# Optimization experiments

Measured on AMD Instinct MI355X. Metric: run time of the kernel, lower is better.

The kernel has to match this reference:

```python
import jax, jax.numpy as jnp
import numpy as np

N, E, R, D = 50000, 640000, 200, 128  # nodes, edges, relations, feat dim (in_feat==out_feat)
EPS = 1e-5  # LayerNorm eps
NEG_SLOPE = 0.01  # F.leaky_relu default

def _xavier(k, shape):
    gain = np.sqrt(2.0)  # calculate_gain('relu')
    std = gain * np.sqrt(2.0 / (shape[0] + shape[1]))
    a = np.sqrt(3.0) * std
    return jax.random.uniform(k, shape, jnp.float32, -a, a)

def setup_inputs() -> dict:
    key = jax.random.key(0)
    ks = jax.random.split(key, 10)
    return {
        "node": jax.random.normal(ks[0], (N, D), jnp.float32),
        "rel": jax.random.normal(ks[1], (R, D), jnp.float32),
        "norm": jax.random.uniform(ks[2], (N, 1), jnp.float32),
        "w_triplet": _xavier(ks[3], (3 * D, D)),
        "w_quad": _xavier(ks[4], (D, D)),
        "loop_weight": _xavier(ks[5], (D, D)),
        "evolve_loop_weight": _xavier(ks[6], (D, D)),
        "src": jax.random.randint(ks[7], (E,), 0, N),
        "dst": jax.random.randint(ks[8], (E,), 0, N),
        "etype": jax.random.randint(ks[9], (E,), 0, R),
    }

def reference(node, rel, norm, w_triplet, w_quad, loop_weight, evolve_loop_weight, src, dst, etype):
    # triplet = cat([h_src, rel_emb, h_dst], 1) @ w_triplet, computed blockwise
    # to avoid materializing the [E, 3D] concat.
    W_s, W_r, W_d = w_triplet[:D], w_triplet[D:2 * D], w_triplet[2 * D:]
    triplet = node[src] @ W_s + rel[etype] @ W_r + node[dst] @ W_d  # [E, D]
    # 'fre' not in edata -> sro_fre is zeros; a_triplet = triplet @ w_quad
    a = jax.nn.leaky_relu(triplet @ w_quad, negative_slope=NEG_SLOPE)  # [E, D]
    # edge_softmax: softmax over incoming edges per destination node, per feature
    a_max = jax.ops.segment_max(a, dst, num_segments=N)
    a_max = jnp.where(jnp.isfinite(a_max), a_max, 0.0)  # empty segments -> -inf
    ex = jnp.exp(a - a_max[dst])
    denom = jax.ops.segment_sum(ex, dst, num_segments=N)
    att = ex / denom[dst]
    # weighted scatter-sum aggregation, then apply_func: h * norm
    h = jax.ops.segment_sum(att * triplet, dst, num_segments=N) * norm  # [N, D]
    # self-loop: evolve_loop_weight for in-degree-0 nodes, loop_weight otherwise
    indeg = jax.ops.segment_sum(jnp.ones((E,), jnp.float32), dst, num_segments=N)
    loop = jnp.where((indeg > 0)[:, None], node @ loop_weight, node @ evolve_loop_weight)
    out = h + loop
    # LayerNorm(elementwise_affine=False)
    mu = jnp.mean(out, axis=-1, keepdims=True)
    var = jnp.var(out, axis=-1, keepdims=True)
    return (out - mu) * jax.lax.rsqrt(var + EPS)
```

## Files before the change

kernel.cpp:

```cpp
#include <hip/hip_runtime.h>
#include <hip/hip_bf16.h>

#define D 128

typedef __attribute__((ext_vector_type(8))) short bf16x8;
typedef __attribute__((ext_vector_type(4))) float f32x4;

__device__ __forceinline__ unsigned short f2bf_bits(float f) {
    union { __hip_bfloat16 h; unsigned short u; } c;
    c.h = __float2bfloat16(f);
    return c.u;
}
__device__ __forceinline__ float bfbits2f(unsigned short u) {
    return __uint_as_float(((unsigned)u) << 16);
}
__device__ __forceinline__ float ldf(const void* p, size_t i, int f32) {
    return f32 ? ((const float*)p)[i] : bfbits2f(((const unsigned short*)p)[i]);
}
__device__ __forceinline__ void unpk(unsigned u, float& a, float& b) {
    a = __uint_as_float(u << 16);
    b = __uint_as_float(u & 0xFFFF0000u);
}

__global__ void init_kernel(const void* node, int* flag, int* a, int n) {
    if (blockIdx.x == 0 && threadIdx.x < 64) {
        int t = threadIdx.x;
        int bad = 0;
        for (int j = 0; j < 4; j++) {
            float v = bfbits2f(((const unsigned short*)node)[t + 64 * j]);
            if (!(fabsf(v) < 1e4f)) bad = 1;
        }
        unsigned long long m = __ballot(bad);
        if (t == 0) *flag = (m != 0ull) ? 1 : 0;
    }
    int i = blockIdx.x * blockDim.x + threadIdx.x;
    int s = gridDim.x * blockDim.x;
    for (int j = i; j < n; j += s) a[j] = 0;
}

__global__ void wq_kernel(const void* w_trip, const void* w_quad,
                          unsigned short* wsqAll, const int* flag) {
    int f32 = *flag;
    int k = blockIdx.x, m = blockIdx.y, t = threadIdx.x;
    float acc = 0.f;
    for (int j = 0; j < D; j++)
        acc += ldf(w_trip, (size_t)m * D * D + (size_t)k * D + j, f32) *
               ldf(w_quad, (size_t)j * D + t, f32);
    wsqAll[m * D * D + k * D + t] = f2bf_bits(acc);
}

__global__ void trans_kernel(const void* wtrip, const void* loopW, const void* evoW,
                             const unsigned short* wsqAll, unsigned short* wT,
                             const int* flag) {
    int j = blockIdx.x;
    int f32 = *flag;
    const void* srcp; size_t base; int isbf;
    switch (j) {
        case 0: srcp = wsqAll; base = 0;         isbf = 1;    break;
        case 1: srcp = wtrip;  base = 0;         isbf = !f32; break;
        case 2: srcp = wsqAll; base = 2 * D * D; isbf = 1;    break;
        case 3: srcp = wtrip;  base = 2 * D * D; isbf = !f32; break;
        case 4: srcp = loopW;  base = 0;         isbf = !f32; break;
        case 5: srcp = evoW;   base = 0;         isbf = !f32; break;
        case 6: srcp = wsqAll; base = D * D;     isbf = 1;    break;
        default: srcp = wtrip; base = D * D;     isbf = !f32; break;
    }
    for (int c = threadIdx.x; c < 1024; c += blockDim.x) {
        int idx = blockIdx.y * 1024 + c;
        int n = idx >> 7, k = idx & 127;
        unsigned short b;
        if (isbf) b = ((const unsigned short*)srcp)[base + (size_t)k * D + n];
        else      b = f2bf_bits(((const float*)srcp)[base + (size_t)k * D + n]);
        wT[(size_t)j * D * D + (size_t)n * D + k] = b;
    }
}

__global__ __launch_bounds__(256) void gemm_kernel(
    const void* __restrict__ node, const void* __restrict__ rel,
    const unsigned short* __restrict__ wT, const int* __restrict__ cnt,
    unsigned* __restrict__ nodeST, unsigned* __restrict__ nodeDT,
    unsigned* __restrict__ relRT, unsigned* __restrict__ loopSel,
    const int* __restrict__ flag, int N, int R, int nodeBlocks) {
    __shared__ __align__(16) unsigned short Wt[D][D + 8];

    int f32 = *flag;
    int bx = blockIdx.x;
    int isRel = bx >= nodeBlocks;
    int jp = isRel ? 3 : blockIdx.y;
    if (isRel && blockIdx.y != 0) return;

    int rows = isRel ? R : N;
    int row0 = (isRel ? bx - nodeBlocks : bx) * 64;
    const void* A = isRel ? rel : node;

    int tid = threadIdx.y * 64 + threadIdx.x;
    int lane = threadIdx.x, wv = threadIdx.y;
    int l16 = lane & 15, quad = lane >> 4;
    int ar = row0 + wv * 16 + l16;
    int ar_c = ar < rows ? ar : rows - 1;

    int qIdx, tIdx;
    unsigned* O = nullptr;
    switch (jp) {
        case 0: qIdx = 0; tIdx = 1; O = nodeST; break;
        case 1: qIdx = 2; tIdx = 3; O = nodeDT; break;
        case 2: qIdx = 4; tIdx = 5; break;
        default: qIdx = 6; tIdx = 7; O = relRT; break;
    }

    bf16x8 af[4];
#pragma unroll
    for (int kk = 0; kk < 4; kk++) {
        int k = kk * 32 + quad * 8;
        if (f32) {
            const float* Af = (const float*)A + (size_t)ar_c * D + k;
#pragma unroll
            for (int j = 0; j < 8; j++) af[kk][j] = (short)f2bf_bits(Af[j]);
        } else {
            af[kk] = *(const bf16x8*)((const unsigned short*)A + (size_t)ar_c * D + k);
        }
    }

    const unsigned short* gQ = wT + (size_t)qIdx * D * D;
    const unsigned short* gT = wT + (size_t)tIdx * D * D;

    bf16x8 wreg[8], wreg2[8];
#pragma unroll
    for (int i = 0; i < 8; i++) {
        int c = tid + i * 256;
        wreg[i] = *(const bf16x8*)(gQ + (c >> 4) * 128 + (c & 15) * 8);
    }

    f32x4 accQ[8], accT[8];
#pragma unroll
    for (int i = 0; i < 8; i++) {
        accQ[i] = (f32x4){0.f, 0.f, 0.f, 0.f};
        accT[i] = (f32x4){0.f, 0.f, 0.f, 0.f};
    }

    for (int pass = 0; pass < 2; pass++) {
#pragma unroll
        for (int i = 0; i < 8; i++) {
            int c = tid + i * 256;
            *(bf16x8*)(&Wt[c >> 4][(c & 15) * 8]) = wreg[i];
        }
        if (pass == 0) {
#pragma unroll
            for (int i = 0; i < 8; i++) {
                int c = tid + i * 256;
                wreg2[i] = *(const bf16x8*)(gT + (c >> 4) * 128 + (c & 15) * 8);
            }
        }
        __syncthreads();
        f32x4* acc = pass ? accT : accQ;
#pragma unroll
        for (int kk = 0; kk < 4; kk++) {
#pragma unroll
            for (int nt = 0; nt < 8; nt++) {
                bf16x8 bfr = *(const bf16x8*)(&Wt[nt * 16 + l16][kk * 32 + quad * 8]);
                acc[nt] = __builtin_amdgcn_mfma_f32_16x16x32_bf16(af[kk], bfr, acc[nt], 0, 0, 0);
            }
        }
        __syncthreads();
#pragma unroll
        for (int i = 0; i < 8; i++) wreg[i] = wreg2[i];
    }

    int cr0 = row0 + wv * 16 + quad * 4;
    int odd = l16 & 1;
    if (jp != 2) {
#pragma unroll
        for (int r = 0; r < 4; r++) {
            int cr = cr0 + r;
#pragma unroll
            for (int nt = 0; nt < 8; nt++) {
                float vQ = accQ[nt][r], vT = accT[nt][r];
                float oQ = __shfl_xor(vQ, 1);
                float oT = __shfl_xor(vT, 1);
                unsigned w;
                if (!odd) w = (unsigned)f2bf_bits(vQ) | ((unsigned)f2bf_bits(oQ) << 16);
                else      w = (unsigned)f2bf_bits(oT) | ((unsigned)f2bf_bits(vT) << 16);
                if (cr < rows) O[(size_t)cr * 128 + nt * 16 + l16] = w;
            }
        }
    } else {
#pragma unroll
        for (int r = 0; r < 4; r++) {
            int cr = cr0 + r;
            int deg = (cr < rows) ? cnt[cr] : 0;
#pragma unroll
            for (int nt = 0; nt < 8; nt++) {
                float vL = accQ[nt][r], vE = accT[nt][r];
                float oL = __shfl_xor(vL, 1);
                float oE = __shfl_xor(vE, 1);
                unsigned wl, we;
                if (!odd) {
                    wl = (unsigned)f2bf_bits(vL) | ((unsigned)f2bf_bits(oL) << 16);
                    we = (unsigned)f2bf_bits(vE) | ((unsigned)f2bf_bits(oE) << 16);
                } else {
                    wl = (unsigned)f2bf_bits(oL) | ((unsigned)f2bf_bits(vL) << 16);
                    we = (unsigned)f2bf_bits(oE) | ((unsigned)f2bf_bits(vE) << 16);
                }
                if (cr < rows && !odd)
                    loopSel[(size_t)cr * 64 + nt * 8 + (l16 >> 1)] = (deg > 0) ? wl : we;
            }
        }
    }
}

__global__ void count_kernel(const int* __restrict__ dst, int* __restrict__ cnt, int E) {
    int e = blockIdx.x * blockDim.x + threadIdx.x;
    if (e < E) atomicAdd(&cnt[dst[e]], 1);
}

__global__ void scan_block(const int* __restrict__ cnt, int* __restrict__ offs,
                           int* __restrict__ part, int N) {
    __shared__ int sh[256];
    int tid = threadIdx.x;
    int i = blockIdx.x * 256 + tid;
    int v = (i < N) ? cnt[i] : 0;
    sh[tid] = v;
    __syncthreads();
    for (int o = 1; o < 256; o <<= 1) {
        int t = (tid >= o) ? sh[tid - o] : 0;
        __syncthreads();
        sh[tid] += t;
        __syncthreads();
    }
    if (i < N) offs[i] = sh[tid] - v;
    if (tid == 255) part[blockIdx.x] = sh[255];
}

__global__ void scan_part(int* __restrict__ part, int nb) {
    __shared__ int sh[256];
    int tid = threadIdx.x;
    int v = (tid < nb) ? part[tid] : 0;
    sh[tid] = v;
    __syncthreads();
    for (int o = 1; o < 256; o <<= 1) {
        int t = (tid >= o) ? sh[tid - o] : 0;
        __syncthreads();
        sh[tid] += t;
        __syncthreads();
    }
    if (tid < nb) part[tid] = sh[tid] - v;
}

__global__ void scan_add(int* __restrict__ offs, const int* __restrict__ part,
                         int N, int E) {
    int i = blockIdx.x * 256 + threadIdx.x;
    if (i < N) offs[i] += part[blockIdx.x];
    if (i == 0) offs[N] = E;
}

__global__ void scatter_kernel(const int* __restrict__ src, const int* __restrict__ dst,
                               const int* __restrict__ et, const int* __restrict__ offs,
                               int* __restrict__ cur, unsigned* __restrict__ ePack, int E) {
    int e = blockIdx.x * blockDim.x + threadIdx.x;
    if (e >= E) return;
    int d = dst[e];
    int pos = offs[d] + atomicAdd(&cur[d], 1);
    ePack[pos] = (unsigned)src[e] | ((unsigned)et[e] << 20);
}

__global__ __launch_bounds__(256) void agg_kernel(
    const int* __restrict__ offs, const unsigned* __restrict__ ePack,
    const uint2* __restrict__ ST, const uint2* __restrict__ RT,
    const uint2* __restrict__ DT, const unsigned* __restrict__ loopSel,
    const void* __restrict__ normv, void* __restrict__ out,
    const int* __restrict__ flag, int N) {
    int n = blockIdx.x * 4 + threadIdx.y;
    if (n >= N) return;
    int f32 = *flag;
    int lane = threadIdx.x;
    int start = offs[n], end = offs[n + 1];
    int deg = end - start;

    unsigned ul = loopSel[(size_t)n * 64 + lane];
    uint2 ud = DT[(size_t)n * 64 + lane];
    float qd0, qd1, td0, td1, acc0, acc1;
    unpk(ud.x, qd0, qd1);
    unpk(ud.y, td0, td1);
    unpk(ul, acc0, acc1);

    float den0 = 0.f, den1 = 0.f, h0 = 0.f, h1 = 0.f;
    for (int e0 = start; e0 < end; e0 += 64) {
        int m = end - e0;
        if (m > 64) m = 64;
        unsigned pk = (lane < m) ? ePack[e0 + lane] : 0u;
        int j = 0;
#define EDGE_LOADS(J, US, UR)                                         \
        unsigned pk_##US = __shfl(pk, (J));                           \
        uint2 US = ST[(size_t)(pk_##US & 0xFFFFFu) * 64 + lane];      \
        uint2 UR = RT[(size_t)(pk_##US >> 20) * 64 + lane];
#define EDGE_MATH(US, UR)                                             \
        {                                                             \
            float qs0, qs1, qr0, qr1, ts0, ts1, tr0, tr1;             \
            unpk(US.x, qs0, qs1); unpk(UR.x, qr0, qr1);               \
            unpk(US.y, ts0, ts1); unpk(UR.y, tr0, tr1);               \
            float q0 = qs0 + qr0 + qd0, q1 = qs1 + qr1 + qd1;         \
            float a0 = q0 > 0.f ? q0 : 0.01f * q0;                    \
            float a1 = q1 > 0.f ? q1 : 0.01f * q1;                    \
            float ex0 = __expf(a0), ex1 = __expf(a1);                 \
            den0 += ex0; den1 += ex1;                                 \
            h0 += ex0 * (ts0 + tr0 + td0);                            \
            h1 += ex1 * (ts1 + tr1 + td1);                            \
        }
        for (; j + 3 < m; j += 4) {
            EDGE_LOADS(j + 0, uA, rA)
            EDGE_LOADS(j + 1, uB, rB)
            EDGE_LOADS(j + 2, uC, rC)
            EDGE_LOADS(j + 3, uD, rD)
            EDGE_MATH(uA, rA)
            EDGE_MATH(uB, rB)
            EDGE_MATH(uC, rC)
            EDGE_MATH(uD, rD)
        }
        for (; j < m; j++) {
            EDGE_LOADS(j, uE, rE)
            EDGE_MATH(uE, rE)
        }
    }

    float x0, x1;
    if (deg > 0) {
        float nrm = ldf(normv, n, f32);
        x0 = h0 / den0 * nrm + acc0;
        x1 = h1 / den1 * nrm + acc1;
    } else {
        x0 = acc0;
        x1 = acc1;
    }

    float s = x0 + x1, ss = x0 * x0 + x1 * x1;
#pragma unroll
    for (int o = 32; o; o >>= 1) {
        s += __shfl_xor(s, o);
        ss += __shfl_xor(ss, o);
    }
    float mu = s * (1.f / 128.f);
    float var = ss * (1.f / 128.f) - mu * mu;
    float rstd = rsqrtf(var + 1e-5f);
    float y0 = (x0 - mu) * rstd, y1 = (x1 - mu) * rstd;

    if (f32) {
        ((float2*)out)[(size_t)n * 64 + lane] = make_float2(y0, y1);
    } else {
        unsigned ob = (unsigned)f2bf_bits(y0) | ((unsigned)f2bf_bits(y1) << 16);
        ((unsigned*)out)[(size_t)n * 64 + lane] = ob;
    }
}

extern "C" void kernel_launch(void* const* d_in, const int* in_sizes, int n_in,
                              void* d_out, int out_size, void* d_ws, size_t ws_size,
                              hipStream_t stream) {
    const void* node = d_in[0];
    const void* rel = d_in[1];
    const void* normv = d_in[2];
    const void* wtrip = d_in[3];
    const void* wquad = d_in[4];
    const void* loopW = d_in[5];
    const void* evoW = d_in[6];
    const int* src = (const int*)d_in[7];
    const int* dst = (const int*)d_in[8];
    const int* et = (const int*)d_in[9];

    int N = in_sizes[0] / D;
    int R = in_sizes[1] / D;
    int E = in_sizes[7];
    int nb = (N + 255) / 256;
    int nodeBlocks = (N + 63) / 64;
    int relBlocks = (R + 63) / 64;

    char* p = (char*)d_ws;
    auto alloc = [&](size_t bytes) -> void* {
        void* r = (void*)p;
        p += (bytes + 255) & ~(size_t)255;
        return r;
    };
    unsigned* nodeST = (unsigned*)alloc((size_t)N * 128 * 4);
    unsigned* nodeDT = (unsigned*)alloc((size_t)N * 128 * 4);
    unsigned* relRT = (unsigned*)alloc((size_t)R * 128 * 4);
    unsigned* loopSel = (unsigned*)alloc((size_t)N * 64 * 4);
    unsigned short* wsqAll = (unsigned short*)alloc((size_t)3 * D * D * 2);
    unsigned short* wT = (unsigned short*)alloc((size_t)8 * D * D * 2);
    int* cnt = (int*)alloc((size_t)2 * N * 4);
    int* offs = (int*)alloc((size_t)(N + 1) * 4);
    int* part = (int*)alloc((size_t)(nb + 1) * 4);
    unsigned* ePack = (unsigned*)alloc((size_t)E * 4);
    int* flag = (int*)alloc(4);

    init_kernel<<<256, 256, 0, stream>>>(node, flag, cnt, 2 * N);
    wq_kernel<<<dim3(D, 3), D, 0, stream>>>(wtrip, wquad, wsqAll, flag);
    trans_kernel<<<dim3(8, 16), 256, 0, stream>>>(wtrip, loopW, evoW, wsqAll, wT, flag);
    count_kernel<<<(E + 255) / 256, 256, 0, stream>>>(dst, cnt, E);
    gemm_kernel<<<dim3(nodeBlocks + relBlocks, 3), dim3(64, 4), 0, stream>>>(
        node, rel, wT, cnt, nodeST, nodeDT, relRT, loopSel, flag, N, R, nodeBlocks);
    scan_block<<<nb, 256, 0, stream>>>(cnt, offs, part, N);
    scan_part<<<1, 256, 0, stream>>>(part, nb);
    scan_add<<<nb, 256, 0, stream>>>(offs, part, N, E);
    scatter_kernel<<<(E + 255) / 256, 256, 0, stream>>>(src, dst, et, offs, cnt + N,
                                                        ePack, E);
    agg_kernel<<<(N + 3) / 4, dim3(64, 4), 0, stream>>>(
        offs, ePack, (const uint2*)nodeST, (const uint2*)relRT, (const uint2*)nodeDT,
        loopSel, normv, d_out, flag, N);
}
```

Baseline: 269.2 us.

## Merge prep kernels, fold scan phases, and fuse edge scatter into GEMM launch

Replaces init, wq, trans and count kernels with a single prep kernel that splits its blocks between weight products, transposes and degree counting. The weight product now writes directly into the transposed layout, and the zeroing moves to a memset. The three-pass scan becomes two passes, with each block reducing the partial sums it needs. The edge scatter runs as extra blocks inside the GEMM launch. Together these cut the number of launches and let independent work overlap. In exchange, some scan work is repeated per block and the GEMM grid carries many idle blocks in the y=0 and y=2 slices.

After: 255.8 us. 1.05x faster.

```diff
diff --git a/kernel.cpp b/kernel.cpp
--- a/kernel.cpp
+++ b/kernel.cpp
@@ -22,57 +22,94 @@
     b = __uint_as_float(u & 0xFFFF0000u);
 }
 
-__global__ void init_kernel(const void* node, int* flag, int* a, int n) {
-    if (blockIdx.x == 0 && threadIdx.x < 64) {
-        int t = threadIdx.x;
-        int bad = 0;
+__global__ __launch_bounds__(256) void prep_kernel(
+    const void* __restrict__ node, const void* __restrict__ wtrip,
+    const void* __restrict__ wquad, const void* __restrict__ loopW,
+    const void* __restrict__ evoW, unsigned short* __restrict__ wT,
+    int* __restrict__ cnt, const int* __restrict__ dst, int* __restrict__ flag,
+    int E) {
+    __shared__ int sflag;
+    int tid = threadIdx.x;
+    int bad = 0;
+    if (tid < 64) {
         for (int j = 0; j < 4; j++) {
-            float v = bfbits2f(((const unsigned short*)node)[t + 64 * j]);
+            float v = bfbits2f(((const unsigned short*)node)[tid + 64 * j]);
             if (!(fabsf(v) < 1e4f)) bad = 1;
         }
-        unsigned long long m = __ballot(bad);
-        if (t == 0) *flag = (m != 0ull) ? 1 : 0;
-    }
-    int i = blockIdx.x * blockDim.x + threadIdx.x;
-    int s = gridDim.x * blockDim.x;
-    for (int j = i; j < n; j += s) a[j] = 0;
-}
-
-__global__ void wq_kernel(const void* w_trip, const void* w_quad,
-                          unsigned short* wsqAll, const int* flag) {
-    int f32 = *flag;
-    int k = blockIdx.x, m = blockIdx.y, t = threadIdx.x;
-    float acc = 0.f;
-    for (int j = 0; j < D; j++)
-        acc += ldf(w_trip, (size_t)m * D * D + (size_t)k * D + j, f32) *
-               ldf(w_quad, (size_t)j * D + t, f32);
-    wsqAll[m * D * D + k * D + t] = f2bf_bits(acc);
-}
-
-__global__ void trans_kernel(const void* wtrip, const void* loopW, const void* evoW,
-                             const unsigned short* wsqAll, unsigned short* wT,
-                             const int* flag) {
-    int j = blockIdx.x;
-    int f32 = *flag;
-    const void* srcp; size_t base; int isbf;
-    switch (j) {
-        case 0: srcp = wsqAll; base = 0;         isbf = 1;    break;
-        case 1: srcp = wtrip;  base = 0;         isbf = !f32; break;
-        case 2: srcp = wsqAll; base = 2 * D * D; isbf = 1;    break;
-        case 3: srcp = wtrip;  base = 2 * D * D; isbf = !f32; break;
-        case 4: srcp = loopW;  base = 0;         isbf = !f32; break;
-        case 5: srcp = evoW;   base = 0;         isbf = !f32; break;
-        case 6: srcp = wsqAll; base = D * D;     isbf = 1;    break;
-        default: srcp = wtrip; base = D * D;     isbf = !f32; break;
-    }
-    for (int c = threadIdx.x; c < 1024; c += blockDim.x) {
-        int idx = blockIdx.y * 1024 + c;
-        int n = idx >> 7, k = idx & 127;
-        unsigned short b;
-        if (isbf) b = ((const unsigned short*)srcp)[base + (size_t)k * D + n];
-        else      b = f2bf_bits(((const float*)srcp)[base + (size_t)k * D + n]);
-        wT[(size_t)j * D * D + (size_t)n * D + k] = b;
-    }
+    }
+    unsigned long long m = __ballot(bad);
+    if (tid == 0) sflag = (m != 0ull) ? 1 : 0;
+    __syncthreads();
+    int f32 = sflag;
+    int bx = blockIdx.x;
+    if (bx == 0 && tid == 0) *flag = f32;
+
+    if (bx < 192) {
+        int unit = bx * 2 + (tid >> 7);
+        int k = unit & 127, mjob = unit >> 7;
+        int t = tid & 127;
+        float acc = 0.f;
+        for (int j = 0; j < D; j++)
+            acc += ldf(wtrip, (size_t)mjob * D * D + (size_t)k * D + j, f32) *
+                   ldf(wquad, (size_t)j * D + t, f32);
+        const int jmap0 = (mjob == 0) ? 0 : (mjob == 1 ? 6 : 2);
+        wT[(size_t)jmap0 * D * D + (size_t)t * D + k] = f2bf_bits(acc);
+    } else if (bx < 272) {
+        int u = bx - 192;
+        int jr = u >> 4, seg = u & 15;
+        const void* srcp; size_t base; int j;
+        switch (jr) {
+            case 0: srcp = wtrip; base = 0;             j = 1; break;
+            case 1: srcp = wtrip; base = 2 * D * D;     j = 3; break;
+            case 2: srcp = loopW; base = 0;             j = 4; break;
+            case 3: srcp = evoW;  base = 0;             j = 5; break;
+            default: srcp = wtrip; base = (size_t)D * D; j = 7; break;
+        }
+        for (int c = tid; c < 1024; c += 256) {
+            int idx = seg * 1024 + c;
+            int n = idx >> 7, k = idx & 127;
+            unsigned short b = f32 ? f2bf_bits(((const float*)srcp)[base + (size_t)k * D + n])
+                                   : ((const unsigned short*)srcp)[base + (size_t)k * D + n];
+            wT[(size_t)j * D * D + (size_t)n * D + k] = b;
+        }
+    } else {
+        int e = (bx - 272) * 256 + tid;
+        if (e < E) atomicAdd(&cnt[dst[e]], 1);
+    }
+}
+
+__global__ void scan_block(const int* __restrict__ cnt, int* __restrict__ offs,
+                           int* __restrict__ part, int N) {
+    __shared__ int sh[256];
+    int tid = threadIdx.x;
+    int i = blockIdx.x * 256 + tid;
+    int v = (i < N) ? cnt[i] : 0;
+    sh[tid] = v;
+    __syncthreads();
+    for (int o = 1; o < 256; o <<= 1) {
+        int t = (tid >= o) ? sh[tid - o] : 0;
+        __syncthreads();
+        sh[tid] += t;
+        __syncthreads();
+    }
+    if (i < N) offs[i] = sh[tid] - v;
+    if (tid == 255) part[blockIdx.x] = sh[255];
+}
+
+__global__ void scan_fix(int* __restrict__ offs, const int* __restrict__ part,
+                         int N, int E) {
+    __shared__ int sh[256];
+    int tid = threadIdx.x, b = blockIdx.x;
+    sh[tid] = (tid < b) ? part[tid] : 0;
+    __syncthreads();
+    for (int o = 128; o; o >>= 1) {
+        if (tid < o) sh[tid] += sh[tid + o];
+        __syncthreads();
+    }
+    int carry = sh[0];
+    int i = b * 256 + tid;
+    if (i < N) offs[i] += carry;
+    if (b == 0 && tid == 0) offs[N] = E;
 }
 
 __global__ __launch_bounds__(256) void gemm_kernel(
@@ -80,20 +117,37 @@
     const unsigned short* __restrict__ wT, const int* __restrict__ cnt,
     unsigned* __restrict__ nodeST, unsigned* __restrict__ nodeDT,
     unsigned* __restrict__ relRT, unsigned* __restrict__ loopSel,
-    const int* __restrict__ flag, int N, int R, int nodeBlocks) {
+    const int* __restrict__ flag, int N, int R, int nodeBlocks,
+    const int* __restrict__ src, const int* __restrict__ dst,
+    const int* __restrict__ et, const int* __restrict__ offs,
+    int* __restrict__ cur, unsigned* __restrict__ ePack, int E) {
     __shared__ __align__(16) unsigned short Wt[D][D + 8];
 
+    int bx = blockIdx.x, by = blockIdx.y;
+    int tid = threadIdx.y * 64 + threadIdx.x;
+    int isRel = 0, jp;
+    if (bx >= nodeBlocks) {
+        if (by == 1) {
+            int e = (bx - nodeBlocks) * 256 + tid;
+            if (e < E) {
+                int d = dst[e];
+                int pos = offs[d] + atomicAdd(&cur[d], 1);
+                ePack[pos] = (unsigned)src[e] | ((unsigned)et[e] << 20);
+            }
+            return;
+        }
+        if (by != 0 || bx - nodeBlocks >= (R + 63) / 64) return;
+        isRel = 1;
+        jp = 3;
+    } else {
+        jp = by;
+    }
+
     int f32 = *flag;
-    int bx = blockIdx.x;
-    int isRel = bx >= nodeBlocks;
-    int jp = isRel ? 3 : blockIdx.y;
-    if (isRel && blockIdx.y != 0) return;
-
     int rows = isRel ? R : N;
     int row0 = (isRel ? bx - nodeBlocks : bx) * 64;
     const void* A = isRel ? rel : node;
 
-    int tid = threadIdx.y * 64 + threadIdx.x;
     int lane = threadIdx.x, wv = threadIdx.y;
     int l16 = lane & 15, quad = lane >> 4;
     int ar = row0 + wv * 16 + l16;
@@ -206,61 +260,6 @@
             }
         }
     }
-}
-
-__global__ void count_kernel(const int* __restrict__ dst, int* __restrict__ cnt, int E) {
-    int e = blockIdx.x * blockDim.x + threadIdx.x;
-    if (e < E) atomicAdd(&cnt[dst[e]], 1);
-}
-
-__global__ void scan_block(const int* __restrict__ cnt, int* __restrict__ offs,
-                           int* __restrict__ part, int N) {
-    __shared__ int sh[256];
-    int tid = threadIdx.x;
-    int i = blockIdx.x * 256 + tid;
-    int v = (i < N) ? cnt[i] : 0;
-    sh[tid] = v;
-    __syncthreads();
-    for (int o = 1; o < 256; o <<= 1) {
-        int t = (tid >= o) ? sh[tid - o] : 0;
-        __syncthreads();
-        sh[tid] += t;
-        __syncthreads();
-    }
-    if (i < N) offs[i] = sh[tid] - v;
-    if (tid == 255) part[blockIdx.x] = sh[255];
-}
-
-__global__ void scan_part(int* __restrict__ part, int nb) {
-    __shared__ int sh[256];
-    int tid = threadIdx.x;
-    int v = (tid < nb) ? part[tid] : 0;
-    sh[tid] = v;
-    __syncthreads();
-    for (int o = 1; o < 256; o <<= 1) {
-        int t = (tid >= o) ? sh[tid - o] : 0;
-        __syncthreads();
-        sh[tid] += t;
-        __syncthreads();
-    }
-    if (tid < nb) part[tid] = sh[tid] - v;
-}
-
-__global__ void scan_add(int* __restrict__ offs, const int* __restrict__ part,
-                         int N, int E) {
-    int i = blockIdx.x * 256 + threadIdx.x;
-    if (i < N) offs[i] += part[blockIdx.x];
-    if (i == 0) offs[N] = E;
-}
-
-__global__ void scatter_kernel(const int* __restrict__ src, const int* __restrict__ dst,
-                               const int* __restrict__ et, const int* __restrict__ offs,
-                               int* __restrict__ cur, unsigned* __restrict__ ePack, int E) {
-    int e = blockIdx.x * blockDim.x + threadIdx.x;
-    if (e >= E) return;
-    int d = dst[e];
-    int pos = offs[d] + atomicAdd(&cur[d], 1);
-    ePack[pos] = (unsigned)src[e] | ((unsigned)et[e] << 20);
 }
 
 __global__ __launch_bounds__(256) void agg_kernel(
@@ -371,6 +370,7 @@
     int nb = (N + 255) / 256;
     int nodeBlocks = (N + 63) / 64;
     int relBlocks = (R + 63) / 64;
+    int scatBlocks = (E + 255) / 256;
 
     char* p = (char*)d_ws;
     auto alloc = [&](size_t bytes) -> void* {
@@ -382,7 +382,6 @@
     unsigned* nodeDT = (unsigned*)alloc((size_t)N * 128 * 4);
     unsigned* relRT = (unsigned*)alloc((size_t)R * 128 * 4);
     unsigned* loopSel = (unsigned*)alloc((size_t)N * 64 * 4);
-    unsigned short* wsqAll = (unsigned short*)alloc((size_t)3 * D * D * 2);
     unsigned short* wT = (unsigned short*)alloc((size_t)8 * D * D * 2);
     int* cnt = (int*)alloc((size_t)2 * N * 4);
     int* offs = (int*)alloc((size_t)(N + 1) * 4);
@@ -390,17 +389,15 @@
     unsigned* ePack = (unsigned*)alloc((size_t)E * 4);
     int* flag = (int*)alloc(4);
 
-    init_kernel<<<256, 256, 0, stream>>>(node, flag, cnt, 2 * N);
-    wq_kernel<<<dim3(D, 3), D, 0, stream>>>(wtrip, wquad, wsqAll, flag);
-    trans_kernel<<<dim3(8, 16), 256, 0, stream>>>(wtrip, loopW, evoW, wsqAll, wT, flag);
-    count_kernel<<<(E + 255) / 256, 256, 0, stream>>>(dst, cnt, E);
-    gemm_kernel<<<dim3(nodeBlocks + relBlocks, 3), dim3(64, 4), 0, stream>>>(
-        node, rel, wT, cnt, nodeST, nodeDT, relRT, loopSel, flag, N, R, nodeBlocks);
+    hipMemsetAsync(cnt, 0, (size_t)2 * N * 4, stream);
+    prep_kernel<<<272 + scatBlocks, 256, 0, stream>>>(
+        node, wtrip, wquad, loopW, evoW, wT, cnt, dst, flag, E);
     scan_block<<<nb, 256, 0, stream>>>(cnt, offs, part, N);
-    scan_part<<<1, 256, 0, stream>>>(part, nb);
-    scan_add<<<nb, 256, 0, stream>>>(offs, part, N, E);
-    scatter_kernel<<<(E + 255) / 256, 256, 0, stream>>>(src, dst, et, offs, cnt + N,
-                                                        ePack, E);
+    scan_fix<<<nb, 256, 0, stream>>>(offs, part, N, E);
+    int xext = nodeBlocks + (scatBlocks > relBlocks ? scatBlocks : relBlocks);
+    gemm_kernel<<<dim3(xext, 3), dim3(64, 4), 0, stream>>>(
+        node, rel, wT, cnt, nodeST, nodeDT, relRT, loopSel, flag, N, R, nodeBlocks,
+        src, dst, et, offs, cnt + N, ePack, E);
     agg_kernel<<<(N + 3) / 4, dim3(64, 4), 0, stream>>>(
         offs, ePack, (const uint2*)nodeST, (const uint2*)relRT, (const uint2*)nodeDT,
         loopSel, normv, d_out, flag, N);
```
